# Performance work log

Hardware: AMD Instinct MI355X
Metric: run time of the kernel (lower is better)

The kernel has to match this reference:

```python
import jax, jax.numpy as jnp
import numpy as np

N_NODES = 100000
N_EDGES = 1600000
D_IN, D_HID, D_OUT = 128, 16, 32


def setup_inputs() -> dict:
    key = jax.random.key(0)
    k1, k2, k3, k4, k5 = jax.random.split(key, 5)
    features = jax.random.normal(k1, (N_NODES, D_IN), dtype=jnp.float32)
    src = jax.random.randint(k2, (N_EDGES,), 0, N_NODES, dtype=jnp.int32)
    dst = jax.random.randint(k3, (N_EDGES,), 0, N_NODES, dtype=jnp.int32)
    # linear layer params (PyTorch Linear: y = x @ W.T + b); store as (in, out)
    s1 = 1.0 / np.sqrt(D_IN)
    s2 = 1.0 / np.sqrt(D_HID)
    W1 = jax.random.uniform(k4, (D_IN, D_HID), minval=-s1, maxval=s1, dtype=jnp.float32)
    b1 = jnp.zeros((D_HID,), dtype=jnp.float32)
    W2 = jax.random.uniform(k5, (D_HID, D_OUT), minval=-s2, maxval=s2, dtype=jnp.float32)
    b2 = jnp.zeros((D_OUT,), dtype=jnp.float32)
    return {"features": features, "src": src, "dst": dst,
            "W1": W1, "b1": b1, "W2": W2, "b2": b2}


def _gcn_layer(h, src, dst, W, b):
    # copy_src + sum: aggregate neighbor (src) features onto dst nodes
    agg = jax.ops.segment_sum(h[src], dst, num_segments=N_NODES)
    return agg @ W + b


def reference(features, src, dst, W1, b1, W2, b2):
    x = jax.nn.relu(_gcn_layer(features, src, dst, W1, b1))
    x = _gcn_layer(x, src, dst, W2, b2)
    return x
```

## Files before the change

kernel.cpp:

```cpp
#include <hip/hip_runtime.h>
#include <hip/hip_bf16.h>

#define N_NODES 100000
#define N_EDGES 1600000
#define D_IN    128
#define D_HID   16
#define D_OUT   32

#define BSHIFT 8
#define BNODES 256
#define NB 391
#define NBPAD 512
#define SCHUNK 4096
#define SBLOCKS 391
#define SLAB 4608
#define NOSTRIDE 257

__device__ inline float bf_lo(unsigned dw) { return __uint_as_float(dw << 16); }
__device__ inline float bf_hi(unsigned dw) { return __uint_as_float(dw & 0xffff0000u); }
__device__ inline unsigned bf_pack(float f0, float f1) {
    union { __hip_bfloat16 h[2]; unsigned u; } pu;
    pu.h[0] = __float2bfloat16(f0);
    pu.h[1] = __float2bfloat16(f1);
    return pu.u;
}
__device__ inline void acc4(float* a, uint2 w) {
    a[0] += bf_lo(w.x); a[1] += bf_hi(w.x);
    a[2] += bf_lo(w.y); a[3] += bf_hi(w.y);
}

__global__ __launch_bounds__(256) void k_mm1(const float* __restrict__ feat,
                                             const float* __restrict__ W1,
                                             unsigned* __restrict__ Yu,
                                             int* __restrict__ cursor) {
    __shared__ float sW[D_IN * D_HID];
    int tid = threadIdx.x, blk = blockIdx.x;
    for (int i = tid; i < D_IN * D_HID; i += 256) sW[i] = W1[i];
    if (tid == 0 && blk < NB) cursor[blk] = blk * SLAB;
    __syncthreads();

    int gid = blk * 256 + tid;
    int n = gid >> 2;
    int jq = gid & 3;
    if (n >= N_NODES) return;

    const float4* f4 = (const float4*)(feat + (size_t)n * D_IN);
    const float4* sW4 = (const float4*)sW;

    float4 acc = make_float4(0.f, 0.f, 0.f, 0.f);
#pragma unroll 8
    for (int kq = 0; kq < 32; ++kq) {
        float4 f = f4[kq];
        int k0 = kq * 4;
        float4 w0 = sW4[(k0 + 0) * 4 + jq];
        float4 w1 = sW4[(k0 + 1) * 4 + jq];
        float4 w2 = sW4[(k0 + 2) * 4 + jq];
        float4 w3 = sW4[(k0 + 3) * 4 + jq];
        acc.x += f.x * w0.x + f.y * w1.x + f.z * w2.x + f.w * w3.x;
        acc.y += f.x * w0.y + f.y * w1.y + f.z * w2.y + f.w * w3.y;
        acc.z += f.x * w0.z + f.y * w1.z + f.z * w2.z + f.w * w3.z;
        acc.w += f.x * w0.w + f.y * w1.w + f.z * w2.w + f.w * w3.w;
    }
    uint2 o;
    o.x = bf_pack(acc.x, acc.y);
    o.y = bf_pack(acc.z, acc.w);
    ((uint2*)(Yu + (size_t)n * 8))[jq] = o;
}

__global__ __launch_bounds__(256) void k_sortscatter(const int* __restrict__ src,
                                                     const int* __restrict__ dst,
                                                     int* __restrict__ cursor,
                                                     unsigned* __restrict__ pairs) {
    __shared__ int hist[NBPAD];
    __shared__ int lbase[NBPAD];
    __shared__ int gbase[NB];
    __shared__ int tscan[256];
    __shared__ unsigned sorted[SCHUNK];
    __shared__ unsigned short bId[SCHUNK];

    int tid = threadIdx.x;
    int base = blockIdx.x * SCHUNK;
    int nval = N_EDGES - base;
    if (nval > SCHUNK) nval = SCHUNK;

    for (int i = tid; i < NBPAD; i += 256) hist[i] = 0;
    __syncthreads();

    int varr[16], barr[16];
#pragma unroll
    for (int k = 0; k < 16; ++k) {
        int e = base + k * 256 + tid;
        if (e < N_EDGES) {
            int s = src[e], d = dst[e];
            varr[k] = (s << BSHIFT) | (d & (BNODES - 1));
            int b = d >> BSHIFT;
            barr[k] = b;
            atomicAdd(&hist[b], 1);
        } else {
            barr[k] = -1;
        }
    }
    __syncthreads();

    int i0 = tid * 2;
    int h0 = hist[i0], h1 = hist[i0 + 1];
    int lsum = h0 + h1;
    tscan[tid] = lsum;
    __syncthreads();
#pragma unroll
    for (int off = 1; off < 256; off <<= 1) {
        int x = (tid >= off) ? tscan[tid - off] : 0;
        __syncthreads();
        tscan[tid] += x;
        __syncthreads();
    }
    int excl = tscan[tid] - lsum;
    lbase[i0 + 0] = excl;
    lbase[i0 + 1] = excl + h0;
    __syncthreads();

    for (int i = tid; i < NB; i += 256) {
        int c = hist[i];
        if (c > 0) gbase[i] = atomicAdd(&cursor[i], c);
    }
    __syncthreads();
    for (int i = tid; i < NBPAD; i += 256) hist[i] = 0;
    __syncthreads();

#pragma unroll
    for (int k = 0; k < 16; ++k) {
        int b = barr[k];
        if (b >= 0) {
            int r = atomicAdd(&hist[b], 1);
            int p = lbase[b] + r;
            sorted[p] = (unsigned)varr[k];
            bId[p] = (unsigned short)b;
        }
    }
    __syncthreads();

    for (int i = tid; i < nval; i += 256) {
        int b = bId[i];
        pairs[gbase[b] + (i - lbase[b])] = sorted[i];
    }
}

__global__ __launch_bounds__(256) void k_nodesort(const int* __restrict__ cursor,
                                                  unsigned* __restrict__ pairs,
                                                  int* __restrict__ node_off) {
    __shared__ unsigned buf[SLAB];
    __shared__ int hist[BNODES];
    __shared__ int cur[BNODES];
    __shared__ int t[256];

    int tid = threadIdx.x, b = blockIdx.x;
    int beg = b * SLAB;
    int cnt = cursor[b] - beg;

    hist[tid] = 0;
    __syncthreads();

    for (int i = tid; i < cnt; i += 256) {
        unsigned p = pairs[beg + i];
        buf[i] = p;
        atomicAdd(&hist[p & (BNODES - 1)], 1);
    }
    __syncthreads();

    int v = hist[tid];
    t[tid] = v;
    __syncthreads();
#pragma unroll
    for (int off = 1; off < 256; off <<= 1) {
        int x = (tid >= off) ? t[tid - off] : 0;
        __syncthreads();
        t[tid] += x;
        __syncthreads();
    }
    int excl = t[tid] - v;
    cur[tid] = excl;
    node_off[b * NOSTRIDE + tid] = beg + excl;
    if (tid == 0) node_off[b * NOSTRIDE + BNODES] = beg + cnt;
    __syncthreads();

    for (int i = tid; i < cnt; i += 256) {
        unsigned p = buf[i];
        int pos = atomicAdd(&cur[p & (BNODES - 1)], 1);
        pairs[beg + pos] = p >> BSHIFT;
    }
}

__global__ __launch_bounds__(256) void k_agg1(const int* __restrict__ node_off,
                                              const unsigned* __restrict__ csr,
                                              const uint2* __restrict__ Yu2,
                                              const float* __restrict__ bias1,
                                              uint2* __restrict__ H1u2) {
    int tid = threadIdx.x;
    int g = tid >> 2, c = tid & 3;
    int n = blockIdx.x * 64 + g;
    if (n >= N_NODES) return;
    int idx = n + (n >> 8);
    int beg = node_off[idx], end = node_off[idx + 1];

    float a[4] = {0.f, 0.f, 0.f, 0.f}, b[4] = {0.f, 0.f, 0.f, 0.f};
    int i = beg;
    for (; i + 7 < end; i += 8) {
        unsigned s0 = csr[i],     s1 = csr[i + 1], s2 = csr[i + 2], s3 = csr[i + 3];
        unsigned s4 = csr[i + 4], s5 = csr[i + 5], s6 = csr[i + 6], s7 = csr[i + 7];
        uint2 w0 = Yu2[(size_t)s0 * 4 + c];
        uint2 w1 = Yu2[(size_t)s1 * 4 + c];
        uint2 w2 = Yu2[(size_t)s2 * 4 + c];
        uint2 w3 = Yu2[(size_t)s3 * 4 + c];
        uint2 w4 = Yu2[(size_t)s4 * 4 + c];
        uint2 w5 = Yu2[(size_t)s5 * 4 + c];
        uint2 w6 = Yu2[(size_t)s6 * 4 + c];
        uint2 w7 = Yu2[(size_t)s7 * 4 + c];
        acc4(a, w0); acc4(b, w1); acc4(a, w2); acc4(b, w3);
        acc4(a, w4); acc4(b, w5); acc4(a, w6); acc4(b, w7);
    }
    for (; i < end; ++i) {
        uint2 w = Yu2[(size_t)csr[i] * 4 + c];
        acc4(a, w);
    }
    float f0 = a[0] + b[0] + bias1[c * 4 + 0];
    float f1 = a[1] + b[1] + bias1[c * 4 + 1];
    float f2 = a[2] + b[2] + bias1[c * 4 + 2];
    float f3 = a[3] + b[3] + bias1[c * 4 + 3];
    uint2 o;
    o.x = bf_pack(fmaxf(f0, 0.f), fmaxf(f1, 0.f));
    o.y = bf_pack(fmaxf(f2, 0.f), fmaxf(f3, 0.f));
    H1u2[(size_t)n * 4 + c] = o;
}

__global__ __launch_bounds__(256) void k_agg2(const int* __restrict__ node_off,
                                              const unsigned* __restrict__ csr,
                                              const uint2* __restrict__ H1u2,
                                              const float* __restrict__ W2,
                                              const float* __restrict__ b2,
                                              float* __restrict__ out) {
    __shared__ float sacc[64][D_HID + 1];
    __shared__ float sW2[D_HID * D_OUT];
    __shared__ float sb2[D_OUT];
    int tid = threadIdx.x;
    for (int i2 = tid; i2 < D_HID * D_OUT; i2 += 256) sW2[i2] = W2[i2];
    if (tid < D_OUT) sb2[tid] = b2[tid];

    int g = tid >> 2, c = tid & 3;
    int n = blockIdx.x * 64 + g;

    float a[4] = {0.f, 0.f, 0.f, 0.f}, b[4] = {0.f, 0.f, 0.f, 0.f};
    if (n < N_NODES) {
        int idx = n + (n >> 8);
        int beg = node_off[idx], end = node_off[idx + 1];
        int i = beg;
        for (; i + 7 < end; i += 8) {
            unsigned s0 = csr[i],     s1 = csr[i + 1], s2 = csr[i + 2], s3 = csr[i + 3];
            unsigned s4 = csr[i + 4], s5 = csr[i + 5], s6 = csr[i + 6], s7 = csr[i + 7];
            uint2 w0 = H1u2[(size_t)s0 * 4 + c];
            uint2 w1 = H1u2[(size_t)s1 * 4 + c];
            uint2 w2 = H1u2[(size_t)s2 * 4 + c];
            uint2 w3 = H1u2[(size_t)s3 * 4 + c];
            uint2 w4 = H1u2[(size_t)s4 * 4 + c];
            uint2 w5 = H1u2[(size_t)s5 * 4 + c];
            uint2 w6 = H1u2[(size_t)s6 * 4 + c];
            uint2 w7 = H1u2[(size_t)s7 * 4 + c];
            acc4(a, w0); acc4(b, w1); acc4(a, w2); acc4(b, w3);
            acc4(a, w4); acc4(b, w5); acc4(a, w6); acc4(b, w7);
        }
        for (; i < end; ++i) {
            uint2 w = H1u2[(size_t)csr[i] * 4 + c];
            acc4(a, w);
        }
    }
    sacc[g][c * 4 + 0] = a[0] + b[0];
    sacc[g][c * 4 + 1] = a[1] + b[1];
    sacc[g][c * 4 + 2] = a[2] + b[2];
    sacc[g][c * 4 + 3] = a[3] + b[3];
    __syncthreads();

    for (int t2 = tid; t2 < 64 * D_OUT; t2 += 256) {
        int gg = t2 >> 5, o = t2 & 31;
        int node = blockIdx.x * 64 + gg;
        if (node < N_NODES) {
            float acc = sb2[o];
#pragma unroll
            for (int j = 0; j < D_HID; ++j)
                acc = fmaf(sacc[gg][j], sW2[j * D_OUT + o], acc);
            out[(size_t)node * D_OUT + o] = acc;
        }
    }
}

extern "C" void kernel_launch(void* const* d_in, const int* in_sizes, int n_in,
                              void* d_out, int out_size, void* d_ws, size_t ws_size,
                              hipStream_t stream) {
    const float* feat = (const float*)d_in[0];
    const int*   src  = (const int*)d_in[1];
    const int*   dst  = (const int*)d_in[2];
    const float* W1   = (const float*)d_in[3];
    const float* b1   = (const float*)d_in[4];
    const float* W2   = (const float*)d_in[5];
    const float* b2   = (const float*)d_in[6];
    float* out = (float*)d_out;

    char* base = (char*)d_ws;
    unsigned* pairs    = (unsigned*)(base);
    unsigned* Yu       = (unsigned*)(base + 7208960);
    unsigned* H1u      = (unsigned*)(base + 10408960);
    int*      cursor   = (int*)(base + 13608960);
    int*      node_off = (int*)(base + 13613056);

    k_mm1        <<<(N_NODES * 4 + 255) / 256, 256, 0, stream>>>(feat, W1, Yu, cursor);
    k_sortscatter<<<SBLOCKS, 256, 0, stream>>>(src, dst, cursor, pairs);
    k_nodesort   <<<NB, 256, 0, stream>>>(cursor, pairs, node_off);
    k_agg1       <<<(N_NODES + 63) / 64, 256, 0, stream>>>(node_off, pairs,
                                                           (const uint2*)Yu, b1,
                                                           (uint2*)H1u);
    k_agg2       <<<(N_NODES + 63) / 64, 256, 0, stream>>>(node_off, pairs,
                                                           (const uint2*)H1u, W2, b2, out);
}
```

Measured before the change: 91.50 us.

## Fuse matmul with edge bucket scatter and widen aggregation gathers to 16 bytes

The first-layer matmul and the edge bucket sort/scatter now run as two disjoint block ranges of one launch, and the cursor initialisation moves into a tiny separate kernel. The aim is for the compute-bound matmul to overlap with the atomic-heavy scatter. The matmul blocks each handle two nodes per thread group to reuse the W1 values loaded from shared memory. Both aggregation kernels switch from four threads per node with 8-byte loads to two threads per node with 16-byte loads, cutting the number of gather instructions. The cost is an extra launch and higher register pressure per thread.

Result: no change. 91.85 us (+0.4%).

```diff
diff --git a/kernel.cpp b/kernel.cpp
--- a/kernel.cpp
+++ b/kernel.cpp
@@ -13,8 +13,17 @@
 #define NBPAD 512
 #define SCHUNK 4096
 #define SBLOCKS 391
+#define MMBLOCKS 782
 #define SLAB 4608
 #define NOSTRIDE 257
+
+#define SS_HIST   0
+#define SS_LBASE  2048
+#define SS_GBASE  4096
+#define SS_TSCAN  5696
+#define SS_SORTED 6720
+#define SS_BID    23104
+#define SS_BYTES  31296
 
 __device__ inline float bf_lo(unsigned dw) { return __uint_as_float(dw << 16); }
 __device__ inline float bf_hi(unsigned dw) { return __uint_as_float(dw & 0xffff0000u); }
@@ -24,124 +33,145 @@
     pu.h[1] = __float2bfloat16(f1);
     return pu.u;
 }
-__device__ inline void acc4(float* a, uint2 w) {
+__device__ inline void acc8(float* a, uint4 w) {
     a[0] += bf_lo(w.x); a[1] += bf_hi(w.x);
     a[2] += bf_lo(w.y); a[3] += bf_hi(w.y);
-}
-
-__global__ __launch_bounds__(256) void k_mm1(const float* __restrict__ feat,
-                                             const float* __restrict__ W1,
-                                             unsigned* __restrict__ Yu,
-                                             int* __restrict__ cursor) {
-    __shared__ float sW[D_IN * D_HID];
+    a[4] += bf_lo(w.z); a[5] += bf_hi(w.z);
+    a[6] += bf_lo(w.w); a[7] += bf_hi(w.w);
+}
+
+__global__ __launch_bounds__(512) void k_init(int* __restrict__ cursor) {
+    int i = threadIdx.x;
+    if (i < NB) cursor[i] = i * SLAB;
+}
+
+__global__ __launch_bounds__(256) void k_fused1(const float* __restrict__ feat,
+                                                const float* __restrict__ W1,
+                                                const int* __restrict__ src,
+                                                const int* __restrict__ dst,
+                                                int* __restrict__ cursor,
+                                                unsigned* __restrict__ pairs,
+                                                unsigned* __restrict__ Yu) {
+    __shared__ char smem[SS_BYTES];
     int tid = threadIdx.x, blk = blockIdx.x;
-    for (int i = tid; i < D_IN * D_HID; i += 256) sW[i] = W1[i];
-    if (tid == 0 && blk < NB) cursor[blk] = blk * SLAB;
-    __syncthreads();
-
-    int gid = blk * 256 + tid;
-    int n = gid >> 2;
-    int jq = gid & 3;
-    if (n >= N_NODES) return;
-
-    const float4* f4 = (const float4*)(feat + (size_t)n * D_IN);
-    const float4* sW4 = (const float4*)sW;
-
-    float4 acc = make_float4(0.f, 0.f, 0.f, 0.f);
-#pragma unroll 8
-    for (int kq = 0; kq < 32; ++kq) {
-        float4 f = f4[kq];
-        int k0 = kq * 4;
-        float4 w0 = sW4[(k0 + 0) * 4 + jq];
-        float4 w1 = sW4[(k0 + 1) * 4 + jq];
-        float4 w2 = sW4[(k0 + 2) * 4 + jq];
-        float4 w3 = sW4[(k0 + 3) * 4 + jq];
-        acc.x += f.x * w0.x + f.y * w1.x + f.z * w2.x + f.w * w3.x;
-        acc.y += f.x * w0.y + f.y * w1.y + f.z * w2.y + f.w * w3.y;
-        acc.z += f.x * w0.z + f.y * w1.z + f.z * w2.z + f.w * w3.z;
-        acc.w += f.x * w0.w + f.y * w1.w + f.z * w2.w + f.w * w3.w;
-    }
-    uint2 o;
-    o.x = bf_pack(acc.x, acc.y);
-    o.y = bf_pack(acc.z, acc.w);
-    ((uint2*)(Yu + (size_t)n * 8))[jq] = o;
-}
-
-__global__ __launch_bounds__(256) void k_sortscatter(const int* __restrict__ src,
-                                                     const int* __restrict__ dst,
-                                                     int* __restrict__ cursor,
-                                                     unsigned* __restrict__ pairs) {
-    __shared__ int hist[NBPAD];
-    __shared__ int lbase[NBPAD];
-    __shared__ int gbase[NB];
-    __shared__ int tscan[256];
-    __shared__ unsigned sorted[SCHUNK];
-    __shared__ unsigned short bId[SCHUNK];
-
-    int tid = threadIdx.x;
-    int base = blockIdx.x * SCHUNK;
-    int nval = N_EDGES - base;
-    if (nval > SCHUNK) nval = SCHUNK;
-
-    for (int i = tid; i < NBPAD; i += 256) hist[i] = 0;
-    __syncthreads();
-
-    int varr[16], barr[16];
-#pragma unroll
-    for (int k = 0; k < 16; ++k) {
-        int e = base + k * 256 + tid;
-        if (e < N_EDGES) {
-            int s = src[e], d = dst[e];
-            varr[k] = (s << BSHIFT) | (d & (BNODES - 1));
-            int b = d >> BSHIFT;
-            barr[k] = b;
-            atomicAdd(&hist[b], 1);
-        } else {
-            barr[k] = -1;
-        }
-    }
-    __syncthreads();
-
-    int i0 = tid * 2;
-    int h0 = hist[i0], h1 = hist[i0 + 1];
-    int lsum = h0 + h1;
-    tscan[tid] = lsum;
-    __syncthreads();
-#pragma unroll
-    for (int off = 1; off < 256; off <<= 1) {
-        int x = (tid >= off) ? tscan[tid - off] : 0;
-        __syncthreads();
-        tscan[tid] += x;
-        __syncthreads();
-    }
-    int excl = tscan[tid] - lsum;
-    lbase[i0 + 0] = excl;
-    lbase[i0 + 1] = excl + h0;
-    __syncthreads();
-
-    for (int i = tid; i < NB; i += 256) {
-        int c = hist[i];
-        if (c > 0) gbase[i] = atomicAdd(&cursor[i], c);
-    }
-    __syncthreads();
-    for (int i = tid; i < NBPAD; i += 256) hist[i] = 0;
-    __syncthreads();
-
-#pragma unroll
-    for (int k = 0; k < 16; ++k) {
-        int b = barr[k];
-        if (b >= 0) {
-            int r = atomicAdd(&hist[b], 1);
-            int p = lbase[b] + r;
-            sorted[p] = (unsigned)varr[k];
-            bId[p] = (unsigned short)b;
-        }
-    }
-    __syncthreads();
-
-    for (int i = tid; i < nval; i += 256) {
-        int b = bId[i];
-        pairs[gbase[b] + (i - lbase[b])] = sorted[i];
+
+    if (blk < SBLOCKS) {
+        int* hist    = (int*)(smem + SS_HIST);
+        int* lbase   = (int*)(smem + SS_LBASE);
+        int* gbase   = (int*)(smem + SS_GBASE);
+        int* tscan   = (int*)(smem + SS_TSCAN);
+        unsigned* sorted = (unsigned*)(smem + SS_SORTED);
+        unsigned short* bId = (unsigned short*)(smem + SS_BID);
+
+        int base = blk * SCHUNK;
+        int nval = N_EDGES - base;
+        if (nval > SCHUNK) nval = SCHUNK;
+
+        for (int i = tid; i < NBPAD; i += 256) hist[i] = 0;
+        __syncthreads();
+
+        int varr[16], barr[16];
+#pragma unroll
+        for (int k = 0; k < 16; ++k) {
+            int e = base + k * 256 + tid;
+            if (e < N_EDGES) {
+                int s = src[e], d = dst[e];
+                varr[k] = (s << BSHIFT) | (d & (BNODES - 1));
+                int b = d >> BSHIFT;
+                barr[k] = b;
+                atomicAdd(&hist[b], 1);
+            } else {
+                barr[k] = -1;
+            }
+        }
+        __syncthreads();
+
+        int i0 = tid * 2;
+        int h0 = hist[i0], h1 = hist[i0 + 1];
+        int lsum = h0 + h1;
+        tscan[tid] = lsum;
+        __syncthreads();
+#pragma unroll
+        for (int off = 1; off < 256; off <<= 1) {
+            int x = (tid >= off) ? tscan[tid - off] : 0;
+            __syncthreads();
+            tscan[tid] += x;
+            __syncthreads();
+        }
+        int excl = tscan[tid] - lsum;
+        lbase[i0 + 0] = excl;
+        lbase[i0 + 1] = excl + h0;
+        __syncthreads();
+
+        for (int i = tid; i < NB; i += 256) {
+            int c = hist[i];
+            if (c > 0) gbase[i] = atomicAdd(&cursor[i], c);
+        }
+        __syncthreads();
+        for (int i = tid; i < NBPAD; i += 256) hist[i] = 0;
+        __syncthreads();
+
+#pragma unroll
+        for (int k = 0; k < 16; ++k) {
+            int b = barr[k];
+            if (b >= 0) {
+                int r = atomicAdd(&hist[b], 1);
+                int p = lbase[b] + r;
+                sorted[p] = (unsigned)varr[k];
+                bId[p] = (unsigned short)b;
+            }
+        }
+        __syncthreads();
+
+        for (int i = tid; i < nval; i += 256) {
+            int b = bId[i];
+            pairs[gbase[b] + (i - lbase[b])] = sorted[i];
+        }
+    } else {
+        float* sW = (float*)smem;
+        for (int i = tid; i < D_IN * D_HID; i += 256) sW[i] = W1[i];
+        __syncthreads();
+
+        int gid = (blk - SBLOCKS) * 256 + tid;
+        int p = gid >> 2;
+        int jq = gid & 3;
+        int n0 = p * 2, n1 = p * 2 + 1;
+        if (n0 >= N_NODES) return;
+        bool has1 = (n1 < N_NODES);
+
+        const float4* f40 = (const float4*)(feat + (size_t)n0 * D_IN);
+        const float4* f41 = (const float4*)(feat + (size_t)n1 * D_IN);
+        const float4* sW4 = (const float4*)sW;
+
+        float4 acc0 = make_float4(0.f, 0.f, 0.f, 0.f);
+        float4 acc1 = make_float4(0.f, 0.f, 0.f, 0.f);
+#pragma unroll 4
+        for (int kq = 0; kq < 32; ++kq) {
+            float4 f0 = f40[kq];
+            float4 f1 = has1 ? f41[kq] : make_float4(0.f, 0.f, 0.f, 0.f);
+            int k0 = kq * 4;
+            float4 w0 = sW4[(k0 + 0) * 4 + jq];
+            float4 w1 = sW4[(k0 + 1) * 4 + jq];
+            float4 w2 = sW4[(k0 + 2) * 4 + jq];
+            float4 w3 = sW4[(k0 + 3) * 4 + jq];
+            acc0.x += f0.x * w0.x + f0.y * w1.x + f0.z * w2.x + f0.w * w3.x;
+            acc0.y += f0.x * w0.y + f0.y * w1.y + f0.z * w2.y + f0.w * w3.y;
+            acc0.z += f0.x * w0.z + f0.y * w1.z + f0.z * w2.z + f0.w * w3.z;
+            acc0.w += f0.x * w0.w + f0.y * w1.w + f0.z * w2.w + f0.w * w3.w;
+            acc1.x += f1.x * w0.x + f1.y * w1.x + f1.z * w2.x + f1.w * w3.x;
+            acc1.y += f1.x * w0.y + f1.y * w1.y + f1.z * w2.y + f1.w * w3.y;
+            acc1.z += f1.x * w0.z + f1.y * w1.z + f1.z * w2.z + f1.w * w3.z;
+            acc1.w += f1.x * w0.w + f1.y * w1.w + f1.z * w2.w + f1.w * w3.w;
+        }
+        uint2 o0, o1;
+        o0.x = bf_pack(acc0.x, acc0.y);
+        o0.y = bf_pack(acc0.z, acc0.w);
+        ((uint2*)(Yu + (size_t)n0 * 8))[jq] = o0;
+        if (has1) {
+            o1.x = bf_pack(acc1.x, acc1.y);
+            o1.y = bf_pack(acc1.z, acc1.w);
+            ((uint2*)(Yu + (size_t)n1 * 8))[jq] = o1;
+        }
     }
 }
 
@@ -192,95 +222,89 @@
 
 __global__ __launch_bounds__(256) void k_agg1(const int* __restrict__ node_off,
                                               const unsigned* __restrict__ csr,
-                                              const uint2* __restrict__ Yu2,
+                                              const uint4* __restrict__ Yu4,
                                               const float* __restrict__ bias1,
-                                              uint2* __restrict__ H1u2) {
+                                              uint4* __restrict__ H1u4) {
     int tid = threadIdx.x;
-    int g = tid >> 2, c = tid & 3;
-    int n = blockIdx.x * 64 + g;
+    int g = tid >> 1, c = tid & 1;
+    int n = blockIdx.x * 128 + g;
     if (n >= N_NODES) return;
     int idx = n + (n >> 8);
     int beg = node_off[idx], end = node_off[idx + 1];
 
-    float a[4] = {0.f, 0.f, 0.f, 0.f}, b[4] = {0.f, 0.f, 0.f, 0.f};
+    float a[8] = {0,0,0,0,0,0,0,0}, b[8] = {0,0,0,0,0,0,0,0};
     int i = beg;
-    for (; i + 7 < end; i += 8) {
-        unsigned s0 = csr[i],     s1 = csr[i + 1], s2 = csr[i + 2], s3 = csr[i + 3];
-        unsigned s4 = csr[i + 4], s5 = csr[i + 5], s6 = csr[i + 6], s7 = csr[i + 7];
-        uint2 w0 = Yu2[(size_t)s0 * 4 + c];
-        uint2 w1 = Yu2[(size_t)s1 * 4 + c];
-        uint2 w2 = Yu2[(size_t)s2 * 4 + c];
-        uint2 w3 = Yu2[(size_t)s3 * 4 + c];
-        uint2 w4 = Yu2[(size_t)s4 * 4 + c];
-        uint2 w5 = Yu2[(size_t)s5 * 4 + c];
-        uint2 w6 = Yu2[(size_t)s6 * 4 + c];
-        uint2 w7 = Yu2[(size_t)s7 * 4 + c];
-        acc4(a, w0); acc4(b, w1); acc4(a, w2); acc4(b, w3);
-        acc4(a, w4); acc4(b, w5); acc4(a, w6); acc4(b, w7);
+    for (; i + 3 < end; i += 4) {
+        unsigned s0 = csr[i], s1 = csr[i + 1], s2 = csr[i + 2], s3 = csr[i + 3];
+        uint4 w0 = Yu4[(size_t)s0 * 2 + c];
+        uint4 w1 = Yu4[(size_t)s1 * 2 + c];
+        uint4 w2 = Yu4[(size_t)s2 * 2 + c];
+        uint4 w3 = Yu4[(size_t)s3 * 2 + c];
+        acc8(a, w0); acc8(b, w1); acc8(a, w2); acc8(b, w3);
     }
     for (; i < end; ++i) {
-        uint2 w = Yu2[(size_t)csr[i] * 4 + c];
-        acc4(a, w);
-    }
-    float f0 = a[0] + b[0] + bias1[c * 4 + 0];
-    float f1 = a[1] + b[1] + bias1[c * 4 + 1];
-    float f2 = a[2] + b[2] + bias1[c * 4 + 2];
-    float f3 = a[3] + b[3] + bias1[c * 4 + 3];
-    uint2 o;
+        uint4 w = Yu4[(size_t)csr[i] * 2 + c];
+        acc8(a, w);
+    }
+    uint4 o;
+    float f0, f1;
+    f0 = a[0] + b[0] + bias1[c * 8 + 0];
+    f1 = a[1] + b[1] + bias1[c * 8 + 1];
     o.x = bf_pack(fmaxf(f0, 0.f), fmaxf(f1, 0.f));
-    o.y = bf_pack(fmaxf(f2, 0.f), fmaxf(f3, 0.f));
-    H1u2[(size_t)n * 4 + c] = o;
+    f0 = a[2] + b[2] + bias1[c * 8 + 2];
+    f1 = a[3] + b[3] + bias1[c * 8 + 3];
+    o.y = bf_pack(fmaxf(f0, 0.f), fmaxf(f1, 0.f));
+    f0 = a[4] + b[4] + bias1[c * 8 + 4];
+    f1 = a[5] + b[5] + bias1[c * 8 + 5];
+    o.z = bf_pack(fmaxf(f0, 0.f), fmaxf(f1, 0.f));
+    f0 = a[6] + b[6] + bias1[c * 8 + 6];
+    f1 = a[7] + b[7] + bias1[c * 8 + 7];
+    o.w = bf_pack(fmaxf(f0, 0.f), fmaxf(f1, 0.f));
+    H1u4[(size_t)n * 2 + c] = o;
 }
 
 __global__ __launch_bounds__(256) void k_agg2(const int* __restrict__ node_off,
                                               const unsigned* __restrict__ csr,
-                                              const uint2* __restrict__ H1u2,
+                                              const uint4* __restrict__ H1u4,
                                               const float* __restrict__ W2,
                                               const float* __restrict__ b2,
                                               float* __restrict__ out) {
-    __shared__ float sacc[64][D_HID + 1];
+    __shared__ float sacc[128][D_HID + 1];
     __shared__ float sW2[D_HID * D_OUT];
     __shared__ float sb2[D_OUT];
     int tid = threadIdx.x;
     for (int i2 = tid; i2 < D_HID * D_OUT; i2 += 256) sW2[i2] = W2[i2];
     if (tid < D_OUT) sb2[tid] = b2[tid];
 
-    int g = tid >> 2, c = tid & 3;
-    int n = blockIdx.x * 64 + g;
-
-    float a[4] = {0.f, 0.f, 0.f, 0.f}, b[4] = {0.f, 0.f, 0.f, 0.f};
+    int g = tid >> 1, c = tid & 1;
+    int n = blockIdx.x * 128 + g;
+
+    float a[8] = {0,0,0,0,0,0,0,0}, b[8] = {0,0,0,0,0,0,0,0};
     if (n < N_NODES) {
         int idx = n + (n >> 8);
         int beg = node_off[idx], end = node_off[idx + 1];
         int i = beg;
-        for (; i + 7 < end; i += 8) {
-            unsigned s0 = csr[i],     s1 = csr[i + 1], s2 = csr[i + 2], s3 = csr[i + 3];
-            unsigned s4 = csr[i + 4], s5 = csr[i + 5], s6 = csr[i + 6], s7 = csr[i + 7];
-            uint2 w0 = H1u2[(size_t)s0 * 4 + c];
-            uint2 w1 = H1u2[(size_t)s1 * 4 + c];
-            uint2 w2 = H1u2[(size_t)s2 * 4 + c];
-            uint2 w3 = H1u2[(size_t)s3 * 4 + c];
-            uint2 w4 = H1u2[(size_t)s4 * 4 + c];
-            uint2 w5 = H1u2[(size_t)s5 * 4 + c];
-            uint2 w6 = H1u2[(size_t)s6 * 4 + c];
-            uint2 w7 = H1u2[(size_t)s7 * 4 + c];
-            acc4(a, w0); acc4(b, w1); acc4(a, w2); acc4(b, w3);
-            acc4(a, w4); acc4(b, w5); acc4(a, w6); acc4(b, w7);
+        for (; i + 3 < end; i += 4) {
+            unsigned s0 = csr[i], s1 = csr[i + 1], s2 = csr[i + 2], s3 = csr[i + 3];
+            uint4 w0 = H1u4[(size_t)s0 * 2 + c];
+            uint4 w1 = H1u4[(size_t)s1 * 2 + c];
+            uint4 w2 = H1u4[(size_t)s2 * 2 + c];
+            uint4 w3 = H1u4[(size_t)s3 * 2 + c];
+            acc8(a, w0); acc8(b, w1); acc8(a, w2); acc8(b, w3);
         }
         for (; i < end; ++i) {
-            uint2 w = H1u2[(size_t)csr[i] * 4 + c];
-            acc4(a, w);
-        }
-    }
-    sacc[g][c * 4 + 0] = a[0] + b[0];
-    sacc[g][c * 4 + 1] = a[1] + b[1];
-    sacc[g][c * 4 + 2] = a[2] + b[2];
-    sacc[g][c * 4 + 3] = a[3] + b[3];
-    __syncthreads();
-
-    for (int t2 = tid; t2 < 64 * D_OUT; t2 += 256) {
+            uint4 w = H1u4[(size_t)csr[i] * 2 + c];
+            acc8(a, w);
+        }
+    }
+#pragma unroll
+    for (int j = 0; j < 8; ++j)
+        sacc[g][c * 8 + j] = a[j] + b[j];
+    __syncthreads();
+
+    for (int t2 = tid; t2 < 128 * D_OUT; t2 += 256) {
         int gg = t2 >> 5, o = t2 & 31;
-        int node = blockIdx.x * 64 + gg;
+        int node = blockIdx.x * 128 + gg;
         if (node < N_NODES) {
             float acc = sb2[o];
 #pragma unroll
@@ -310,12 +334,13 @@
     int*      cursor   = (int*)(base + 13608960);
     int*      node_off = (int*)(base + 13613056);
 
-    k_mm1        <<<(N_NODES * 4 + 255) / 256, 256, 0, stream>>>(feat, W1, Yu, cursor);
-    k_sortscatter<<<SBLOCKS, 256, 0, stream>>>(src, dst, cursor, pairs);
-    k_nodesort   <<<NB, 256, 0, stream>>>(cursor, pairs, node_off);
-    k_agg1       <<<(N_NODES + 63) / 64, 256, 0, stream>>>(node_off, pairs,
-                                                           (const uint2*)Yu, b1,
-                                                           (uint2*)H1u);
-    k_agg2       <<<(N_NODES + 63) / 64, 256, 0, stream>>>(node_off, pairs,
-                                                           (const uint2*)H1u, W2, b2, out);
-}
+    k_init  <<<1, 512, 0, stream>>>(cursor);
+    k_fused1<<<SBLOCKS + MMBLOCKS, 256, 0, stream>>>(feat, W1, src, dst,
+                                                     cursor, pairs, Yu);
+    k_nodesort<<<NB, 256, 0, stream>>>(cursor, pairs, node_off);
+    k_agg1  <<<(N_NODES + 127) / 128, 256, 0, stream>>>(node_off, pairs,
+                                                        (const uint4*)Yu, b1,
+                                                        (uint4*)H1u);
+    k_agg2  <<<(N_NODES + 127) / 128, 256, 0, stream>>>(node_off, pairs,
+                                                        (const uint4*)H1u, W2, b2, out);
+}
```

## Fuse edge bucket scatter and first matmul into one heterogeneous kernel launch

Applied to the files above, without the earlier changes.

Merges the first-layer feature matmul and the edge bucket sort/scatter into a single launch, where the first blocks do the scatter and the rest do the matmul. Cursor initialization moves to a memset, and the cursors become relative counts, so the matmul blocks no longer need to run before the scatter. This lets the two independent stages overlap on the GPU and removes one kernel boundary. In exchange it adds a memset launch, and both block types share one larger shared memory allocation, which may reduce occupancy for the matmul blocks.

New measurement: 89.73 us. Within noise of the previous version (-1.9%).

```diff
diff --git a/kernel.cpp b/kernel.cpp
--- a/kernel.cpp
+++ b/kernel.cpp
@@ -13,8 +13,17 @@
 #define NBPAD 512
 #define SCHUNK 4096
 #define SBLOCKS 391
+#define MMBLOCKS 1563
 #define SLAB 4608
 #define NOSTRIDE 257
+
+#define SS_HIST   0
+#define SS_LBASE  2048
+#define SS_GBASE  4096
+#define SS_TSCAN  5696
+#define SS_SORTED 6720
+#define SS_BID    23104
+#define SS_BYTES  31296
 
 __device__ inline float bf_lo(unsigned dw) { return __uint_as_float(dw << 16); }
 __device__ inline float bf_hi(unsigned dw) { return __uint_as_float(dw & 0xffff0000u); }
@@ -29,119 +38,119 @@
     a[2] += bf_lo(w.y); a[3] += bf_hi(w.y);
 }
 
-__global__ __launch_bounds__(256) void k_mm1(const float* __restrict__ feat,
-                                             const float* __restrict__ W1,
-                                             unsigned* __restrict__ Yu,
-                                             int* __restrict__ cursor) {
-    __shared__ float sW[D_IN * D_HID];
+__global__ __launch_bounds__(256) void k_fused1(const float* __restrict__ feat,
+                                                const float* __restrict__ W1,
+                                                const int* __restrict__ src,
+                                                const int* __restrict__ dst,
+                                                int* __restrict__ cursor,
+                                                unsigned* __restrict__ pairs,
+                                                unsigned* __restrict__ Yu) {
+    __shared__ __align__(16) char smem[SS_BYTES];
     int tid = threadIdx.x, blk = blockIdx.x;
-    for (int i = tid; i < D_IN * D_HID; i += 256) sW[i] = W1[i];
-    if (tid == 0 && blk < NB) cursor[blk] = blk * SLAB;
-    __syncthreads();
-
-    int gid = blk * 256 + tid;
-    int n = gid >> 2;
-    int jq = gid & 3;
-    if (n >= N_NODES) return;
-
-    const float4* f4 = (const float4*)(feat + (size_t)n * D_IN);
-    const float4* sW4 = (const float4*)sW;
-
-    float4 acc = make_float4(0.f, 0.f, 0.f, 0.f);
+
+    if (blk < SBLOCKS) {
+        int* hist    = (int*)(smem + SS_HIST);
+        int* lbase   = (int*)(smem + SS_LBASE);
+        int* gbase   = (int*)(smem + SS_GBASE);
+        int* tscan   = (int*)(smem + SS_TSCAN);
+        unsigned* sorted = (unsigned*)(smem + SS_SORTED);
+        unsigned short* bId = (unsigned short*)(smem + SS_BID);
+
+        int base = blk * SCHUNK;
+        int nval = N_EDGES - base;
+        if (nval > SCHUNK) nval = SCHUNK;
+
+        for (int i = tid; i < NBPAD; i += 256) hist[i] = 0;
+        __syncthreads();
+
+        int varr[16], barr[16];
+#pragma unroll
+        for (int k = 0; k < 16; ++k) {
+            int e = base + k * 256 + tid;
+            if (e < N_EDGES) {
+                int s = src[e], d = dst[e];
+                varr[k] = (s << BSHIFT) | (d & (BNODES - 1));
+                int b = d >> BSHIFT;
+                barr[k] = b;
+                atomicAdd(&hist[b], 1);
+            } else {
+                barr[k] = -1;
+            }
+        }
+        __syncthreads();
+
+        int i0 = tid * 2;
+        int h0 = hist[i0], h1 = hist[i0 + 1];
+        int lsum = h0 + h1;
+        tscan[tid] = lsum;
+        __syncthreads();
+#pragma unroll
+        for (int off = 1; off < 256; off <<= 1) {
+            int x = (tid >= off) ? tscan[tid - off] : 0;
+            __syncthreads();
+            tscan[tid] += x;
+            __syncthreads();
+        }
+        int excl = tscan[tid] - lsum;
+        lbase[i0 + 0] = excl;
+        lbase[i0 + 1] = excl + h0;
+        __syncthreads();
+
+        for (int i = tid; i < NB; i += 256) {
+            int c = hist[i];
+            if (c > 0) gbase[i] = i * SLAB + atomicAdd(&cursor[i], c);
+        }
+        __syncthreads();
+        for (int i = tid; i < NBPAD; i += 256) hist[i] = 0;
+        __syncthreads();
+
+#pragma unroll
+        for (int k = 0; k < 16; ++k) {
+            int b = barr[k];
+            if (b >= 0) {
+                int r = atomicAdd(&hist[b], 1);
+                int p = lbase[b] + r;
+                sorted[p] = (unsigned)varr[k];
+                bId[p] = (unsigned short)b;
+            }
+        }
+        __syncthreads();
+
+        for (int i = tid; i < nval; i += 256) {
+            int b = bId[i];
+            pairs[gbase[b] + (i - lbase[b])] = sorted[i];
+        }
+    } else {
+        float* sW = (float*)smem;
+        for (int i = tid; i < D_IN * D_HID; i += 256) sW[i] = W1[i];
+        __syncthreads();
+
+        int gid = (blk - SBLOCKS) * 256 + tid;
+        int n = gid >> 2;
+        int jq = gid & 3;
+        if (n >= N_NODES) return;
+
+        const float4* f4 = (const float4*)(feat + (size_t)n * D_IN);
+        const float4* sW4 = (const float4*)sW;
+
+        float4 acc = make_float4(0.f, 0.f, 0.f, 0.f);
 #pragma unroll 8
-    for (int kq = 0; kq < 32; ++kq) {
-        float4 f = f4[kq];
-        int k0 = kq * 4;
-        float4 w0 = sW4[(k0 + 0) * 4 + jq];
-        float4 w1 = sW4[(k0 + 1) * 4 + jq];
-        float4 w2 = sW4[(k0 + 2) * 4 + jq];
-        float4 w3 = sW4[(k0 + 3) * 4 + jq];
-        acc.x += f.x * w0.x + f.y * w1.x + f.z * w2.x + f.w * w3.x;
-        acc.y += f.x * w0.y + f.y * w1.y + f.z * w2.y + f.w * w3.y;
-        acc.z += f.x * w0.z + f.y * w1.z + f.z * w2.z + f.w * w3.z;
-        acc.w += f.x * w0.w + f.y * w1.w + f.z * w2.w + f.w * w3.w;
-    }
-    uint2 o;
-    o.x = bf_pack(acc.x, acc.y);
-    o.y = bf_pack(acc.z, acc.w);
-    ((uint2*)(Yu + (size_t)n * 8))[jq] = o;
-}
-
-__global__ __launch_bounds__(256) void k_sortscatter(const int* __restrict__ src,
-                                                     const int* __restrict__ dst,
-                                                     int* __restrict__ cursor,
-                                                     unsigned* __restrict__ pairs) {
-    __shared__ int hist[NBPAD];
-    __shared__ int lbase[NBPAD];
-    __shared__ int gbase[NB];
-    __shared__ int tscan[256];
-    __shared__ unsigned sorted[SCHUNK];
-    __shared__ unsigned short bId[SCHUNK];
-
-    int tid = threadIdx.x;
-    int base = blockIdx.x * SCHUNK;
-    int nval = N_EDGES - base;
-    if (nval > SCHUNK) nval = SCHUNK;
-
-    for (int i = tid; i < NBPAD; i += 256) hist[i] = 0;
-    __syncthreads();
-
-    int varr[16], barr[16];
-#pragma unroll
-    for (int k = 0; k < 16; ++k) {
-        int e = base + k * 256 + tid;
-        if (e < N_EDGES) {
-            int s = src[e], d = dst[e];
-            varr[k] = (s << BSHIFT) | (d & (BNODES - 1));
-            int b = d >> BSHIFT;
-            barr[k] = b;
-            atomicAdd(&hist[b], 1);
-        } else {
-            barr[k] = -1;
-        }
-    }
-    __syncthreads();
-
-    int i0 = tid * 2;
-    int h0 = hist[i0], h1 = hist[i0 + 1];
-    int lsum = h0 + h1;
-    tscan[tid] = lsum;
-    __syncthreads();
-#pragma unroll
-    for (int off = 1; off < 256; off <<= 1) {
-        int x = (tid >= off) ? tscan[tid - off] : 0;
-        __syncthreads();
-        tscan[tid] += x;
-        __syncthreads();
-    }
-    int excl = tscan[tid] - lsum;
-    lbase[i0 + 0] = excl;
-    lbase[i0 + 1] = excl + h0;
-    __syncthreads();
-
-    for (int i = tid; i < NB; i += 256) {
-        int c = hist[i];
-        if (c > 0) gbase[i] = atomicAdd(&cursor[i], c);
-    }
-    __syncthreads();
-    for (int i = tid; i < NBPAD; i += 256) hist[i] = 0;
-    __syncthreads();
-
-#pragma unroll
-    for (int k = 0; k < 16; ++k) {
-        int b = barr[k];
-        if (b >= 0) {
-            int r = atomicAdd(&hist[b], 1);
-            int p = lbase[b] + r;
-            sorted[p] = (unsigned)varr[k];
-            bId[p] = (unsigned short)b;
-        }
-    }
-    __syncthreads();
-
-    for (int i = tid; i < nval; i += 256) {
-        int b = bId[i];
-        pairs[gbase[b] + (i - lbase[b])] = sorted[i];
+        for (int kq = 0; kq < 32; ++kq) {
+            float4 f = f4[kq];
+            int k0 = kq * 4;
+            float4 w0 = sW4[(k0 + 0) * 4 + jq];
+            float4 w1 = sW4[(k0 + 1) * 4 + jq];
+            float4 w2 = sW4[(k0 + 2) * 4 + jq];
+            float4 w3 = sW4[(k0 + 3) * 4 + jq];
+            acc.x += f.x * w0.x + f.y * w1.x + f.z * w2.x + f.w * w3.x;
+            acc.y += f.x * w0.y + f.y * w1.y + f.z * w2.y + f.w * w3.y;
+            acc.z += f.x * w0.z + f.y * w1.z + f.z * w2.z + f.w * w3.z;
+            acc.w += f.x * w0.w + f.y * w1.w + f.z * w2.w + f.w * w3.w;
+        }
+        uint2 o;
+        o.x = bf_pack(acc.x, acc.y);
+        o.y = bf_pack(acc.z, acc.w);
+        ((uint2*)(Yu + (size_t)n * 8))[jq] = o;
     }
 }
 
@@ -155,7 +164,7 @@
 
     int tid = threadIdx.x, b = blockIdx.x;
     int beg = b * SLAB;
-    int cnt = cursor[b] - beg;
+    int cnt = cursor[b];
 
     hist[tid] = 0;
     __syncthreads();
@@ -310,12 +319,14 @@
     int*      cursor   = (int*)(base + 13608960);
     int*      node_off = (int*)(base + 13613056);
 
-    k_mm1        <<<(N_NODES * 4 + 255) / 256, 256, 0, stream>>>(feat, W1, Yu, cursor);
-    k_sortscatter<<<SBLOCKS, 256, 0, stream>>>(src, dst, cursor, pairs);
-    k_nodesort   <<<NB, 256, 0, stream>>>(cursor, pairs, node_off);
-    k_agg1       <<<(N_NODES + 63) / 64, 256, 0, stream>>>(node_off, pairs,
-                                                           (const uint2*)Yu, b1,
-                                                           (uint2*)H1u);
-    k_agg2       <<<(N_NODES + 63) / 64, 256, 0, stream>>>(node_off, pairs,
-                                                           (const uint2*)H1u, W2, b2, out);
-}
+    hipMemsetAsync(cursor, 0, NB * sizeof(int), stream);
+
+    k_fused1  <<<SBLOCKS + MMBLOCKS, 256, 0, stream>>>(feat, W1, src, dst,
+                                                       cursor, pairs, Yu);
+    k_nodesort<<<NB, 256, 0, stream>>>(cursor, pairs, node_off);
+    k_agg1    <<<(N_NODES + 63) / 64, 256, 0, stream>>>(node_off, pairs,
+                                                        (const uint2*)Yu, b1,
+                                                        (uint2*)H1u);
+    k_agg2    <<<(N_NODES + 63) / 64, 256, 0, stream>>>(node_off, pairs,
+                                                        (const uint2*)H1u, W2, b2, out);
+}
```
